# Optimization experiments

Hardware: AMD Instinct MI355X
Metric: run time of the kernel (lower is better)

Reference implementation:

```python
import jax, jax.numpy as jnp
import numpy as np

HEADS = 4
DIM_HEAD = 32
SCALE = DIM_HEAD ** -0.5
EPS = 1e-5


def setup_inputs() -> dict:
    key = jax.random.key(0)
    ks = jax.random.split(key, 5)
    b, c, h, w = 32, 256, 64, 64
    hidden = HEADS * DIM_HEAD  # 128
    return {
        "x": jax.random.normal(ks[0], (b, c, h, w), dtype=jnp.float32),
        "Wqkv": jax.random.normal(ks[1], (3 * hidden, c), dtype=jnp.float32) * 0.05,
        "bqkv": jax.random.normal(ks[2], (3 * hidden,), dtype=jnp.float32) * 0.05,
        "Wout": jax.random.normal(ks[3], (c, hidden), dtype=jnp.float32) * 0.05,
        "bout": jax.random.normal(ks[4], (c,), dtype=jnp.float32) * 0.05,
        "gamma": jnp.ones((c,), dtype=jnp.float32),
        "beta": jnp.zeros((c,), dtype=jnp.float32),
    }


def reference(x, Wqkv, bqkv, Wout, bout, gamma, beta):
    b, c, h, w = x.shape
    n = h * w
    # 1x1 conv == per-pixel linear: [b,c,h,w] x [3*hidden,c] -> [b,3*hidden,h,w]
    qkv = jnp.einsum('bchw,oc->bohw', x, Wqkv) + bqkv[None, :, None, None]
    q, k, v = jnp.split(qkv, 3, axis=1)
    # b (heads dh) x y -> b heads dh n
    q = q.reshape(b, HEADS, DIM_HEAD, n)
    k = k.reshape(b, HEADS, DIM_HEAD, n)
    v = v.reshape(b, HEADS, DIM_HEAD, n)
    q = jax.nn.softmax(q, axis=-2) * SCALE  # softmax over dim_head axis
    k = jax.nn.softmax(k, axis=-2)
    context = jnp.einsum('bhdn,bhen->bhde', k, v)   # [b,h,dh,dh]
    out = jnp.einsum('bhde,bhdn->bhen', context, q)  # [b,h,dh,n]
    out = out.reshape(b, HEADS * DIM_HEAD, h, w)
    # 1x1 conv projection back to dim
    out = jnp.einsum('bchw,oc->bohw', out, Wout) + bout[None, :, None, None]
    # GroupNorm(1, dim): normalize over (C,H,W) per sample, affine per channel
    mu = jnp.mean(out, axis=(1, 2, 3), keepdims=True)
    var = jnp.var(out, axis=(1, 2, 3), keepdims=True)
    out = (out - mu) * jax.lax.rsqrt(var + EPS)
    return out * gamma[None, :, None, None] + beta[None, :, None, None]
```

## Files before the change

kernel.cpp:

```cpp
#include <hip/hip_runtime.h>
#include <math.h>


#define NPIX 4096
#define SCALE 0.17677669529663687f

typedef __bf16 bf16;
typedef __bf16 bf16x4 __attribute__((ext_vector_type(4)));
typedef __bf16 bf16x8 __attribute__((ext_vector_type(8)));
typedef float  f32x4  __attribute__((ext_vector_type(4)));

__global__ __launch_bounds__(256) void k0_convert(
    const float* __restrict__ Wqkv, const float* __restrict__ Wout,
    bf16* __restrict__ wqkv_bf, bf16* __restrict__ wout_bf)
{
    int i = blockIdx.x * 256 + threadIdx.x;
    if (i < 98304) wqkv_bf[i] = (bf16)Wqkv[i];
    else           wout_bf[i - 98304] = (bf16)Wout[i - 98304];
}

__global__ __launch_bounds__(256, 3) void k1_qkv(
    const float* __restrict__ x, const bf16* __restrict__ wqkv_bf,
    const float* __restrict__ bqkv, bf16* __restrict__ q_wsT,
    bf16* __restrict__ part)
{
    __shared__ __align__(16) bf16 sm[18432];
    bf16* xT = sm;

    const int blk  = blockIdx.x;
    const int b    = blk >> 6;
    const int n0   = (blk & 63) << 6;
    const int tid  = threadIdx.x;
    const int lane = tid & 63;
    const int s    = __builtin_amdgcn_readfirstlane(tid >> 6);
    const int m16  = lane & 15;
    const int quad = lane >> 4;

    const float* xb = x + (size_t)b * (256 * NPIX) + n0;
    {
        const int px  = tid & 63;
        const int cq0 = tid >> 6;
        float vv[16][4];
        #pragma unroll
        for (int it = 0; it < 16; ++it) {
            const float* xp = xb + (size_t)(cq0 + 4*it) * 4 * NPIX + px;
            vv[it][0] = xp[0];
            vv[it][1] = xp[NPIX];
            vv[it][2] = xp[2*NPIX];
            vv[it][3] = xp[3*NPIX];
        }
        __builtin_amdgcn_sched_barrier(0);
        #pragma unroll
        for (int it = 0; it < 16; ++it) {
            int cq = cq0 + 4*it;
            int gp = (cq >> 1) ^ (px & 7);
            bf16x4 pk = { (bf16)vv[it][0], (bf16)vv[it][1],
                          (bf16)vv[it][2], (bf16)vv[it][3] };
            *(bf16x4*)&xT[px*256 + gp*8 + (cq & 1)*4] = pk;
        }
    }
    __syncthreads();

    {
        f32x4 qacc[2][4] = {};
        for (int kc = 0; kc < 8; ++kc) {
            bf16x8 bfr[4];
            #pragma unroll
            for (int nt = 0; nt < 4; ++nt) {
                int px = nt*16 + m16;
                int gp = (kc*4 + quad) ^ (px & 7);
                bfr[nt] = *(const bf16x8*)&xT[px*256 + gp*8];
            }
            #pragma unroll
            for (int mt = 0; mt < 2; ++mt) {
                int row = s*32 + mt*16 + m16;
                bf16x8 afr = *(const bf16x8*)&wqkv_bf[(size_t)row*256 + kc*32 + quad*8];
                #pragma unroll
                for (int nt = 0; nt < 4; ++nt)
                    qacc[mt][nt] = __builtin_amdgcn_mfma_f32_16x16x32_bf16(afr, bfr[nt], qacc[mt][nt], 0, 0, 0);
            }
        }
        float bq[8];
        #pragma unroll
        for (int j = 0; j < 8; ++j)
            bq[j] = bqkv[s*32 + (j >> 2)*16 + quad*4 + (j & 3)];

        #pragma unroll
        for (int nt = 0; nt < 4; ++nt) {
            float v[8]; float mx = -1e30f;
            #pragma unroll
            for (int j = 0; j < 8; ++j) { v[j] = qacc[j>>2][nt][j&3] + bq[j]; mx = fmaxf(mx, v[j]); }
            mx = fmaxf(mx, __shfl_xor(mx, 16));
            mx = fmaxf(mx, __shfl_xor(mx, 32));
            float sum = 0.f;
            #pragma unroll
            for (int j = 0; j < 8; ++j) { v[j] = __expf(v[j] - mx); sum += v[j]; }
            sum += __shfl_xor(sum, 16);
            sum += __shfl_xor(sum, 32);
            float rs = SCALE / sum;
            size_t rowb = (size_t)(b*4096 + n0 + nt*16 + m16) * 128;
            #pragma unroll
            for (int mt = 0; mt < 2; ++mt) {
                bf16x4 pk = { (bf16)(v[mt*4+0]*rs), (bf16)(v[mt*4+1]*rs),
                              (bf16)(v[mt*4+2]*rs), (bf16)(v[mt*4+3]*rs) };
                *(bf16x4*)&q_wsT[rowb + s*32 + mt*16 + quad*4] = pk;
            }
        }
    }

    f32x4 acc[4][4] = {};
    for (int kc = 0; kc < 8; ++kc) {
        bf16x8 bfr[4];
        #pragma unroll
        for (int nt = 0; nt < 4; ++nt) {
            int px = nt*16 + m16;
            int gp = (kc*4 + quad) ^ (px & 7);
            bfr[nt] = *(const bf16x8*)&xT[px*256 + gp*8];
        }
        #pragma unroll
        for (int mt = 0; mt < 4; ++mt) {
            int row = 128 + (mt >> 1)*128 + s*32 + (mt & 1)*16 + m16;
            bf16x8 afr = *(const bf16x8*)&wqkv_bf[(size_t)row*256 + kc*32 + quad*8];
            #pragma unroll
            for (int nt = 0; nt < 4; ++nt)
                acc[mt][nt] = __builtin_amdgcn_mfma_f32_16x16x32_bf16(afr, bfr[nt], acc[mt][nt], 0, 0, 0);
        }
    }

    float bk[8], bv[8];
    #pragma unroll
    for (int j = 0; j < 8; ++j) {
        int rr = (j >> 2)*16 + quad*4 + (j & 3);
        bk[j] = bqkv[128 + s*32 + rr];
        bv[j] = bqkv[256 + s*32 + rr];
    }

    __syncthreads();
    bf16* kl = sm + s*2304;
    bf16* vl = sm + 9216 + s*2304;
    #pragma unroll
    for (int nt = 0; nt < 4; ++nt) {
        float v[8]; float mx = -1e30f;
        #pragma unroll
        for (int j = 0; j < 8; ++j) { v[j] = acc[j>>2][nt][j&3] + bk[j]; mx = fmaxf(mx, v[j]); }
        mx = fmaxf(mx, __shfl_xor(mx, 16));
        mx = fmaxf(mx, __shfl_xor(mx, 32));
        float sum = 0.f;
        #pragma unroll
        for (int j = 0; j < 8; ++j) { v[j] = __expf(v[j] - mx); sum += v[j]; }
        sum += __shfl_xor(sum, 16);
        sum += __shfl_xor(sum, 32);
        float rs = 1.f / sum;
        #pragma unroll
        for (int j = 0; j < 8; ++j) {
            int d  = (j>>2)*16 + quad*4 + (j&3);
            int px = nt*16 + m16;
            kl[d*72 + px] = (bf16)(v[j] * rs);
            vl[d*72 + px] = (bf16)(acc[2 + (j>>2)][nt][j&3] + bv[j]);
        }
    }
    __syncthreads();

    f32x4 cacc[2][2] = {};
    #pragma unroll
    for (int ks = 0; ks < 2; ++ks) {
        bf16x8 ak[2], bvv[2];
        #pragma unroll
        for (int mt = 0; mt < 2; ++mt)
            ak[mt] = *(const bf16x8*)&kl[(mt*16 + m16)*72 + ks*32 + quad*8];
        #pragma unroll
        for (int nt = 0; nt < 2; ++nt)
            bvv[nt] = *(const bf16x8*)&vl[(nt*16 + m16)*72 + ks*32 + quad*8];
        #pragma unroll
        for (int mt = 0; mt < 2; ++mt)
            #pragma unroll
            for (int nt = 0; nt < 2; ++nt)
                cacc[mt][nt] = __builtin_amdgcn_mfma_f32_16x16x32_bf16(ak[mt], bvv[nt], cacc[mt][nt], 0, 0, 0);
    }
    bf16* pdst = part + (size_t)blk * 4096 + s*1024;
    #pragma unroll
    for (int mt = 0; mt < 2; ++mt)
        #pragma unroll
        for (int nt = 0; nt < 2; ++nt)
            #pragma unroll
            for (int r = 0; r < 4; ++r)
                pdst[(mt*16 + quad*4 + r)*32 + nt*16 + m16] = (bf16)cacc[mt][nt][r];
}

__global__ __launch_bounds__(256) void k2_reduce(
    const bf16* __restrict__ part, bf16* __restrict__ ctxT_bf)
{
    int i = blockIdx.x * 256 + threadIdx.x;
    int b = i >> 12, r = i & 4095;
    const bf16* p = part + (size_t)b * 64 * 4096 + r;
    float sum = 0.f;
    #pragma unroll 8
    for (int j = 0; j < 64; ++j) sum += (float)p[(size_t)j * 4096];
    int h = r >> 10, d = (r >> 5) & 31, e = r & 31;
    ctxT_bf[(size_t)((b*4 + h)*32 + e)*32 + d] = (bf16)sum;
}

__global__ __launch_bounds__(256, 4) void k3_out(
    const bf16* __restrict__ q_wsT, const bf16* __restrict__ ctxT_bf,
    const bf16* __restrict__ wout_bf, const float* __restrict__ bout,
    float* __restrict__ out, float* __restrict__ gstats)
{
    __shared__ __align__(16) bf16 attnT[8192];
    __shared__ float red[512];
    const int blk  = blockIdx.x;
    const int b    = blk >> 6;
    const int n0   = (blk & 63) << 6;
    const int tid  = threadIdx.x;
    const int lane = tid & 63;
    const int s    = __builtin_amdgcn_readfirstlane(tid >> 6);
    const int m16  = lane & 15;
    const int quad = lane >> 4;

    f32x4 aacc[2][4] = {};
    {
        bf16x8 afr[2], bfr[4];
        const bf16* ctxs = ctxT_bf + (size_t)(b*4 + s) * 1024;
        #pragma unroll
        for (int mt = 0; mt < 2; ++mt)
            afr[mt] = *(const bf16x8*)&ctxs[(mt*16 + m16)*32 + quad*8];
        const bf16* qb = q_wsT + (size_t)(b*4096 + n0) * 128 + s*32;
        #pragma unroll
        for (int nt = 0; nt < 4; ++nt)
            bfr[nt] = *(const bf16x8*)&qb[(size_t)(nt*16 + m16)*128 + quad*8];
        #pragma unroll
        for (int mt = 0; mt < 2; ++mt)
            #pragma unroll
            for (int nt = 0; nt < 4; ++nt)
                aacc[mt][nt] = __builtin_amdgcn_mfma_f32_16x16x32_bf16(afr[mt], bfr[nt], aacc[mt][nt], 0, 0, 0);
    }

    #pragma unroll
    for (int mt = 0; mt < 2; ++mt)
        #pragma unroll
        for (int nt = 0; nt < 4; ++nt) {
            int p   = nt*16 + m16;
            int chb = s*32 + mt*16 + quad*4;
            int gp  = (chb >> 3) ^ m16;
            bf16x4 pk = { (bf16)aacc[mt][nt][0], (bf16)aacc[mt][nt][1],
                          (bf16)aacc[mt][nt][2], (bf16)aacc[mt][nt][3] };
            *(bf16x4*)&attnT[p*128 + gp*8 + (quad & 1)*4] = pk;
        }
    __syncthreads();

    float ls = 0.f, lss = 0.f;
    float* ob = out + ((size_t)b*256 + s*64) * NPIX + n0;
    #pragma unroll 1
    for (int h = 0; h < 2; ++h) {
        f32x4 acc[2][4] = {};
        const bf16* wb = wout_bf + (size_t)(s*64 + h*32) * 128;
        for (int kc = 0; kc < 4; ++kc) {
            bf16x8 wfr[2], xfr[4];
            #pragma unroll
            for (int mt = 0; mt < 2; ++mt)
                wfr[mt] = *(const bf16x8*)&wb[(size_t)(mt*16 + m16)*128 + kc*32 + quad*8];
            #pragma unroll
            for (int nt = 0; nt < 4; ++nt) {
                int p  = nt*16 + m16;
                int gp = (kc*4 + quad) ^ m16;
                xfr[nt] = *(const bf16x8*)&attnT[p*128 + gp*8];
            }
            #pragma unroll
            for (int mt = 0; mt < 2; ++mt)
                #pragma unroll
                for (int nt = 0; nt < 4; ++nt)
                    acc[mt][nt] = __builtin_amdgcn_mfma_f32_16x16x32_bf16(wfr[mt], xfr[nt], acc[mt][nt], 0, 0, 0);
        }

        #pragma unroll
        for (int mt = 0; mt < 2; ++mt) {
            #pragma unroll
            for (int r = 0; r < 4; ++r) {
                int o = h*32 + mt*16 + quad*4 + r;
                float bo = bout[s*64 + o];
                #pragma unroll
                for (int nt = 0; nt < 4; ++nt) {
                    float v = acc[mt][nt][r] + bo;
                    ob[(size_t)o*NPIX + nt*16 + m16] = v;
                    ls += v; lss += v*v;
                }
            }
        }
    }

    red[tid] = ls; red[256 + tid] = lss;
    __syncthreads();
    for (int off = 128; off > 0; off >>= 1) {
        if (tid < off) {
            red[tid]       += red[tid + off];
            red[256 + tid] += red[256 + tid + off];
        }
        __syncthreads();
    }
    if (tid == 0) {
        atomicAdd(&gstats[b],      red[0]);
        atomicAdd(&gstats[32 + b], red[256]);
    }
}

__global__ __launch_bounds__(256) void k5_norm(
    float* __restrict__ out, const float* __restrict__ gstats,
    const float* __restrict__ gamma, const float* __restrict__ beta)
{
    const float inv_cnt = 1.0f / 1048576.0f;
    for (size_t gid = (size_t)blockIdx.x * 256 + threadIdx.x;
         gid < 8388608; gid += (size_t)gridDim.x * 256) {
        size_t base = gid * 4;
        int b = (int)(base >> 20);
        int o = (int)((base >> 12) & 255);
        float m   = gstats[b]      * inv_cnt;
        float var = gstats[32 + b] * inv_cnt - m*m;
        float inv = rsqrtf(var + 1e-5f);
        float a = inv * gamma[o];
        float c = beta[o] - m * a;
        float4 v = ((float4*)out)[gid];
        v.x = v.x * a + c; v.y = v.y * a + c;
        v.z = v.z * a + c; v.w = v.w * a + c;
        ((float4*)out)[gid] = v;
    }
}

extern "C" void kernel_launch(void* const* d_in, const int* in_sizes, int n_in,
                              void* d_out, int out_size, void* d_ws, size_t ws_size,
                              hipStream_t stream) {
    const float* x     = (const float*)d_in[0];
    const float* Wqkv  = (const float*)d_in[1];
    const float* bqkv  = (const float*)d_in[2];
    const float* Wout  = (const float*)d_in[3];
    const float* bout  = (const float*)d_in[4];
    const float* gamma = (const float*)d_in[5];
    const float* beta  = (const float*)d_in[6];
    float* out = (float*)d_out;
    float* ws  = (float*)d_ws;

    bf16*  q_wsT   = (bf16*)ws;
    bf16*  wqkv_bf = (bf16*)(ws + 8388608);
    bf16*  wout_bf = (bf16*)(ws + 8437760);
    bf16*  ctxT_bf = (bf16*)(ws + 8454144);
    bf16*  part    = (bf16*)(ws + 16777216);
    float* gstats  = ws + 25165824;

    hipMemsetAsync(gstats, 0, 64 * sizeof(float), stream);
    k0_convert<<<512,  256, 0, stream>>>(Wqkv, Wout, wqkv_bf, wout_bf);
    k1_qkv    <<<2048, 256, 0, stream>>>(x, wqkv_bf, bqkv, q_wsT, part);
    k2_reduce <<<512,  256, 0, stream>>>(part, ctxT_bf);
    k3_out    <<<2048, 256, 0, stream>>>(q_wsT, ctxT_bf, wout_bf, bout, out, gstats);
    k5_norm   <<<4096, 256, 0, stream>>>(out, gstats, gamma, beta);
}
```

Measured before the change: 386.6 us.

## Widen k3 output tile to 128 pixels and raise k1 occupancy

k3_out now processes 128 pixels per block instead of 64, in two halves of the ctx×q MFMA pass. The Wout projection loop is restructured to 16-row output chunks across 8 pixel tiles, so each Wout fragment is reused across more pixels and half as many blocks are launched. k1_qkv's launch bound rises from 3 to 4 waves per SIMD, and the sched_barrier after the x loads is dropped, which may cost registers or change how loads interleave. The k5_norm grid is doubled, which only works if that kernel's indexing tolerates it.

```diff
diff --git a/kernel.cpp b/kernel.cpp
--- a/kernel.cpp
+++ b/kernel.cpp
@@ -19,7 +19,7 @@
     else           wout_bf[i - 98304] = (bf16)Wout[i - 98304];
 }
 
-__global__ __launch_bounds__(256, 3) void k1_qkv(
+__global__ __launch_bounds__(256, 4) void k1_qkv(
     const float* __restrict__ x, const bf16* __restrict__ wqkv_bf,
     const float* __restrict__ bqkv, bf16* __restrict__ q_wsT,
     bf16* __restrict__ part)
@@ -49,7 +49,6 @@
             vv[it][2] = xp[2*NPIX];
             vv[it][3] = xp[3*NPIX];
         }
-        __builtin_amdgcn_sched_barrier(0);
         #pragma unroll
         for (int it = 0; it < 16; ++it) {
             int cq = cq0 + 4*it;
@@ -205,84 +204,82 @@
     const bf16* __restrict__ wout_bf, const float* __restrict__ bout,
     float* __restrict__ out, float* __restrict__ gstats)
 {
-    __shared__ __align__(16) bf16 attnT[8192];
+    __shared__ __align__(16) bf16 attnT[16384];
     __shared__ float red[512];
     const int blk  = blockIdx.x;
-    const int b    = blk >> 6;
-    const int n0   = (blk & 63) << 6;
+    const int b    = blk >> 5;
+    const int n0   = (blk & 31) << 7;
     const int tid  = threadIdx.x;
     const int lane = tid & 63;
     const int s    = __builtin_amdgcn_readfirstlane(tid >> 6);
     const int m16  = lane & 15;
     const int quad = lane >> 4;
 
-    f32x4 aacc[2][4] = {};
-    {
-        bf16x8 afr[2], bfr[4];
-        const bf16* ctxs = ctxT_bf + (size_t)(b*4 + s) * 1024;
-        #pragma unroll
-        for (int mt = 0; mt < 2; ++mt)
-            afr[mt] = *(const bf16x8*)&ctxs[(mt*16 + m16)*32 + quad*8];
-        const bf16* qb = q_wsT + (size_t)(b*4096 + n0) * 128 + s*32;
-        #pragma unroll
-        for (int nt = 0; nt < 4; ++nt)
-            bfr[nt] = *(const bf16x8*)&qb[(size_t)(nt*16 + m16)*128 + quad*8];
+    const bf16* ctxs = ctxT_bf + (size_t)(b*4 + s) * 1024;
+    const bf16* qb   = q_wsT + (size_t)(b*4096 + n0) * 128 + s*32;
+    bf16x8 afr[2];
+    #pragma unroll
+    for (int mt = 0; mt < 2; ++mt)
+        afr[mt] = *(const bf16x8*)&ctxs[(mt*16 + m16)*32 + quad*8];
+
+    #pragma unroll 1
+    for (int h2 = 0; h2 < 2; ++h2) {
+        f32x4 aacc[2][4] = {};
+        bf16x8 bfr[4];
+        #pragma unroll
+        for (int nt = 0; nt < 4; ++nt) {
+            int p = (h2*4 + nt)*16 + m16;
+            bfr[nt] = *(const bf16x8*)&qb[(size_t)p*128 + quad*8];
+        }
         #pragma unroll
         for (int mt = 0; mt < 2; ++mt)
             #pragma unroll
             for (int nt = 0; nt < 4; ++nt)
                 aacc[mt][nt] = __builtin_amdgcn_mfma_f32_16x16x32_bf16(afr[mt], bfr[nt], aacc[mt][nt], 0, 0, 0);
-    }
-
-    #pragma unroll
-    for (int mt = 0; mt < 2; ++mt)
-        #pragma unroll
-        for (int nt = 0; nt < 4; ++nt) {
-            int p   = nt*16 + m16;
-            int chb = s*32 + mt*16 + quad*4;
-            int gp  = (chb >> 3) ^ m16;
-            bf16x4 pk = { (bf16)aacc[mt][nt][0], (bf16)aacc[mt][nt][1],
-                          (bf16)aacc[mt][nt][2], (bf16)aacc[mt][nt][3] };
-            *(bf16x4*)&attnT[p*128 + gp*8 + (quad & 1)*4] = pk;
-        }
+
+        #pragma unroll
+        for (int mt = 0; mt < 2; ++mt)
+            #pragma unroll
+            for (int nt = 0; nt < 4; ++nt) {
+                int p   = (h2*4 + nt)*16 + m16;
+                int chb = s*32 + mt*16 + quad*4;
+                int gp  = (chb >> 3) ^ m16;
+                bf16x4 pk = { (bf16)aacc[mt][nt][0], (bf16)aacc[mt][nt][1],
+                              (bf16)aacc[mt][nt][2], (bf16)aacc[mt][nt][3] };
+                *(bf16x4*)&attnT[p*128 + gp*8 + (quad & 1)*4] = pk;
+            }
+    }
     __syncthreads();
 
     float ls = 0.f, lss = 0.f;
     float* ob = out + ((size_t)b*256 + s*64) * NPIX + n0;
     #pragma unroll 1
-    for (int h = 0; h < 2; ++h) {
-        f32x4 acc[2][4] = {};
-        const bf16* wb = wout_bf + (size_t)(s*64 + h*32) * 128;
+    for (int qh = 0; qh < 4; ++qh) {
+        f32x4 acc[8] = {};
+        const bf16* wb = wout_bf + (size_t)(s*64 + qh*16) * 128;
         for (int kc = 0; kc < 4; ++kc) {
-            bf16x8 wfr[2], xfr[4];
-            #pragma unroll
-            for (int mt = 0; mt < 2; ++mt)
-                wfr[mt] = *(const bf16x8*)&wb[(size_t)(mt*16 + m16)*128 + kc*32 + quad*8];
-            #pragma unroll
-            for (int nt = 0; nt < 4; ++nt) {
+            bf16x8 wfr = *(const bf16x8*)&wb[(size_t)m16*128 + kc*32 + quad*8];
+            bf16x8 xfr[8];
+            #pragma unroll
+            for (int nt = 0; nt < 8; ++nt) {
                 int p  = nt*16 + m16;
                 int gp = (kc*4 + quad) ^ m16;
                 xfr[nt] = *(const bf16x8*)&attnT[p*128 + gp*8];
             }
             #pragma unroll
-            for (int mt = 0; mt < 2; ++mt)
-                #pragma unroll
-                for (int nt = 0; nt < 4; ++nt)
-                    acc[mt][nt] = __builtin_amdgcn_mfma_f32_16x16x32_bf16(wfr[mt], xfr[nt], acc[mt][nt], 0, 0, 0);
-        }
-
-        #pragma unroll
-        for (int mt = 0; mt < 2; ++mt) {
-            #pragma unroll
-            for (int r = 0; r < 4; ++r) {
-                int o = h*32 + mt*16 + quad*4 + r;
-                float bo = bout[s*64 + o];
-                #pragma unroll
-                for (int nt = 0; nt < 4; ++nt) {
-                    float v = acc[mt][nt][r] + bo;
-                    ob[(size_t)o*NPIX + nt*16 + m16] = v;
-                    ls += v; lss += v*v;
-                }
+            for (int nt = 0; nt < 8; ++nt)
+                acc[nt] = __builtin_amdgcn_mfma_f32_16x16x32_bf16(wfr, xfr[nt], acc[nt], 0, 0, 0);
+        }
+
+        #pragma unroll
+        for (int r = 0; r < 4; ++r) {
+            int o = qh*16 + quad*4 + r;
+            float bo = bout[s*64 + o];
+            #pragma unroll
+            for (int nt = 0; nt < 8; ++nt) {
+                float v = acc[nt][r] + bo;
+                ob[(size_t)o*NPIX + nt*16 + m16] = v;
+                ls += v; lss += v*v;
             }
         }
     }
@@ -348,6 +345,6 @@
     k0_convert<<<512,  256, 0, stream>>>(Wqkv, Wout, wqkv_bf, wout_bf);
     k1_qkv    <<<2048, 256, 0, stream>>>(x, wqkv_bf, bqkv, q_wsT, part);
     k2_reduce <<<512,  256, 0, stream>>>(part, ctxT_bf);
-    k3_out    <<<2048, 256, 0, stream>>>(q_wsT, ctxT_bf, wout_bf, bout, out, gstats);
-    k5_norm   <<<4096, 256, 0, stream>>>(out, gstats, gamma, beta);
-}
+    k3_out    <<<1024, 256, 0, stream>>>(q_wsT, ctxT_bf, wout_bf, bout, out, gstats);
+    k5_norm   <<<8192, 256, 0, stream>>>(out, gstats, gamma, beta);
+}
```

New measurement: 421.5 us. 9.0% more time.
